# Kernel tuning notes

Hardware: AMD Instinct MI355X
Metric: run time of the kernel (lower is better)

## Reference

```python
import jax, jax.numpy as jnp
import numpy as np


def setup_inputs() -> dict:
    key = jax.random.key(0)
    N, E, LENGTH, DIM = 50000, 800000, 128, 128
    k1, k2, k3 = jax.random.split(key, 3)
    x = jax.random.normal(k1, (N, LENGTH), dtype=jnp.float32)
    edge_index = jax.random.randint(k2, (2, E), 0, N, dtype=jnp.int32)
    W = jax.random.normal(k3, (LENGTH, DIM), dtype=jnp.float32) / np.sqrt(LENGTH).astype(np.float32)
    b = jnp.zeros((DIM,), dtype=jnp.float32)
    return {"x": x, "edge_index": edge_index, "W": W, "b": b, "length": LENGTH, "dim": DIM}


def reference(x, edge_index, W, b, length, dim):
    # GCNConv(length, dim) with default add_self_loops + symmetric normalization,
    # then ReLU and softmax over the feature axis (dim=1).
    N = x.shape[0]
    src, dst = edge_index[0], edge_index[1]  # messages flow src -> dst (PyG source_to_target)
    loop = jnp.arange(N, dtype=src.dtype)
    src = jnp.concatenate([src, loop])
    dst = jnp.concatenate([dst, loop])
    # degree (incl. self-loops) computed on destination nodes, as in PyG gcn_norm
    deg = jax.ops.segment_sum(jnp.ones(dst.shape, dtype=x.dtype), dst, num_segments=N)
    dinv = jnp.where(deg > 0, jax.lax.rsqrt(deg), 0.0)
    norm = dinv[src] * dinv[dst]  # [E+N]
    xw = x @ W  # [N, dim] -- transform before propagate (in >= out here)
    msgs = xw[src] * norm[:, None]  # [E+N, dim] gather + scale
    out = jax.ops.segment_sum(msgs, dst, num_segments=N) + b  # scatter-add
    out = jax.nn.relu(out)
    return jax.nn.softmax(out, axis=1)
```

## Files before the change

### kernel.cpp

```cpp
#include <hip/hip_runtime.h>
#include <hip/hip_bf16.h>


#define KDIM 128
#define CAP 48

__device__ __forceinline__ unsigned short f2bf(float f) {
    union { float f; unsigned u; } v; v.f = f;
    unsigned r = v.u + 0x7fff + ((v.u >> 16) & 1);
    return (unsigned short)(r >> 16);
}
__device__ __forceinline__ float bflo(unsigned u) {
    union { unsigned u; float f; } v; v.u = u << 16; return v.f;
}
__device__ __forceinline__ float bfhi(unsigned u) {
    union { unsigned u; float f; } v; v.u = u & 0xffff0000u; return v.f;
}

__global__ __launch_bounds__(256) void fused_k(const float* __restrict__ x,
                                               const float* __restrict__ W,
                                               const int* __restrict__ src,
                                               const int* __restrict__ dst,
                                               int* __restrict__ degi,
                                               unsigned short* __restrict__ csr,
                                               unsigned short* __restrict__ xwh,
                                               int N, int E, int GB) {
    __shared__ float Xl[128 * 17];
    __shared__ float Wl[16 * 132];

    const int tid = threadIdx.x;

    if ((int)blockIdx.x >= GB) {
        int e = ((int)blockIdx.x - GB) * 256 + tid;
        if (e < E) {
            int d = dst[e];
            int s = src[e];
            int pos = atomicAdd(&degi[d], 1);
            if (pos < CAP) csr[d * CAP + pos] = (unsigned short)s;
        }
        return;
    }

    const int tx = tid & 15;
    const int ty = tid >> 4;
    const int rbase = (int)blockIdx.x * 128;

    float acc[8][8];
#pragma unroll
    for (int j = 0; j < 8; ++j)
#pragma unroll
        for (int c = 0; c < 8; ++c) acc[j][c] = 0.f;

    for (int kc = 0; kc < KDIM; kc += 16) {
#pragma unroll
        for (int i = 0; i < 2; ++i) {
            int p = tid + 256 * i;
            int row = p >> 2;
            int c4 = p & 3;
            int gr = rbase + row;
            float4 v = make_float4(0.f, 0.f, 0.f, 0.f);
            if (gr < N) v = *(const float4*)(&x[(size_t)gr * KDIM + kc + c4 * 4]);
            float* dp = &Xl[row * 17 + c4 * 4];
            dp[0] = v.x; dp[1] = v.y; dp[2] = v.z; dp[3] = v.w;
        }
#pragma unroll
        for (int i = 0; i < 2; ++i) {
            int p = tid + 256 * i;
            int k = p >> 5;
            int c4 = p & 31;
            float4 v = *(const float4*)(&W[(size_t)(kc + k) * KDIM + c4 * 4]);
            *(float4*)(&Wl[k * 132 + c4 * 4]) = v;
        }
        __syncthreads();

#pragma unroll
        for (int k = 0; k < 16; ++k) {
            float xr[8];
#pragma unroll
            for (int j = 0; j < 8; ++j) xr[j] = Xl[(ty * 8 + j) * 17 + k];
            float4 w0 = *(const float4*)(&Wl[k * 132 + tx * 4]);
            float4 w1 = *(const float4*)(&Wl[k * 132 + tx * 4 + 64]);
#pragma unroll
            for (int j = 0; j < 8; ++j) {
                acc[j][0] += xr[j] * w0.x; acc[j][1] += xr[j] * w0.y;
                acc[j][2] += xr[j] * w0.z; acc[j][3] += xr[j] * w0.w;
                acc[j][4] += xr[j] * w1.x; acc[j][5] += xr[j] * w1.y;
                acc[j][6] += xr[j] * w1.z; acc[j][7] += xr[j] * w1.w;
            }
        }
        __syncthreads();
    }

#pragma unroll
    for (int j = 0; j < 8; ++j) {
        int gr = rbase + ty * 8 + j;
        if (gr < N) {
            ushort4 o0, o1;
            o0.x = f2bf(acc[j][0]); o0.y = f2bf(acc[j][1]);
            o0.z = f2bf(acc[j][2]); o0.w = f2bf(acc[j][3]);
            o1.x = f2bf(acc[j][4]); o1.y = f2bf(acc[j][5]);
            o1.z = f2bf(acc[j][6]); o1.w = f2bf(acc[j][7]);
            *(ushort4*)(&xwh[(size_t)gr * KDIM + tx * 4]) = o0;
            *(ushort4*)(&xwh[(size_t)gr * KDIM + tx * 4 + 64]) = o1;
        }
    }
}

__global__ __launch_bounds__(256) void gather_k(const unsigned short* __restrict__ xwh,
                                                const unsigned short* __restrict__ csr,
                                                const int* __restrict__ degi,
                                                const float* __restrict__ b,
                                                float* __restrict__ out, int N) {
    int node = (blockIdx.x * blockDim.x + threadIdx.x) >> 6;
    if (node >= N) return;
    int lane = threadIdx.x & 63;
    int h = lane >> 4;
    int c = lane & 15;

    int cnt = degi[node];
    int ccnt = min(cnt, CAP);
    float dn = rsqrtf((float)(cnt + 1));

    float a[8];
#pragma unroll
    for (int i = 0; i < 8; ++i) a[i] = 0.f;

    if (h == 0) {
        float sn = dn * dn;
        uint4 u = *(const uint4*)(&xwh[(size_t)node * KDIM + c * 8]);
        float4 b0 = *(const float4*)(&b[c * 8]);
        float4 b1 = *(const float4*)(&b[c * 8 + 4]);
        a[0] = bflo(u.x) * sn + b0.x; a[1] = bfhi(u.x) * sn + b0.y;
        a[2] = bflo(u.y) * sn + b0.z; a[3] = bfhi(u.y) * sn + b0.w;
        a[4] = bflo(u.z) * sn + b1.x; a[5] = bfhi(u.z) * sn + b1.y;
        a[6] = bflo(u.w) * sn + b1.z; a[7] = bfhi(u.w) * sn + b1.w;
    }

    int s_l = 0;
    float w_l = 0.f;
    if (lane < ccnt) {
        s_l = csr[(size_t)node * CAP + lane];
        w_l = rsqrtf((float)(degi[s_l] + 1));
    }

    int kmax = (ccnt + 3) >> 2;
#pragma unroll 4
    for (int k = 0; k < kmax; ++k) {
        int idx = 4 * k + h;
        int s = __shfl(s_l, idx);
        float nv = __shfl(w_l, idx) * dn;
        uint4 u = *(const uint4*)(&xwh[(size_t)s * KDIM + c * 8]);
        a[0] += bflo(u.x) * nv; a[1] += bfhi(u.x) * nv;
        a[2] += bflo(u.y) * nv; a[3] += bfhi(u.y) * nv;
        a[4] += bflo(u.z) * nv; a[5] += bfhi(u.z) * nv;
        a[6] += bflo(u.w) * nv; a[7] += bfhi(u.w) * nv;
    }

#pragma unroll
    for (int off = 16; off <= 32; off <<= 1) {
#pragma unroll
        for (int i = 0; i < 8; ++i) a[i] += __shfl_xor(a[i], off);
    }

    float mx = -1e30f;
#pragma unroll
    for (int i = 0; i < 8; ++i) {
        a[i] = fmaxf(a[i], 0.f);
        mx = fmaxf(mx, a[i]);
    }
#pragma unroll
    for (int off = 1; off < 16; off <<= 1) mx = fmaxf(mx, __shfl_xor(mx, off));
    float e[8], s = 0.f;
#pragma unroll
    for (int i = 0; i < 8; ++i) {
        e[i] = __expf(a[i] - mx);
        s += e[i];
    }
#pragma unroll
    for (int off = 1; off < 16; off <<= 1) s += __shfl_xor(s, off);
    float rs = 1.0f / s;
    if (h == 0) {
        float4 o0 = make_float4(e[0] * rs, e[1] * rs, e[2] * rs, e[3] * rs);
        float4 o1 = make_float4(e[4] * rs, e[5] * rs, e[6] * rs, e[7] * rs);
        *(float4*)(&out[(size_t)node * KDIM + c * 8]) = o0;
        *(float4*)(&out[(size_t)node * KDIM + c * 8 + 4]) = o1;
    }
}

extern "C" void kernel_launch(void* const* d_in, const int* in_sizes, int n_in,
                              void* d_out, int out_size, void* d_ws, size_t ws_size,
                              hipStream_t stream) {
    const float* x  = (const float*)d_in[0];
    const int*   ei = (const int*)d_in[1];
    const float* W  = (const float*)d_in[2];
    const float* b  = (const float*)d_in[3];

    const int N = in_sizes[0] / KDIM;
    const int E = in_sizes[1] / 2;
    const int* src = ei;
    const int* dst = ei + E;

    unsigned short* xwh  = (unsigned short*)d_ws;
    int*            degi = (int*)(xwh + (size_t)N * KDIM);
    unsigned short* csr  = (unsigned short*)(degi + N);
    float*          out  = (float*)d_out;

    hipMemsetAsync(degi, 0, (size_t)N * sizeof(int), stream);

    const int GB = (N + 127) / 128;
    const int FB = (E + 255) / 256;
    fused_k<<<GB + FB, 256, 0, stream>>>(x, W, src, dst, degi, csr, xwh, N, E, GB);

    gather_k<<<(N + 3) / 4, 256, 0, stream>>>(xwh, csr, degi, b, out, N);
}
```

Before: 164.5 us.

## Use bf16 MFMA for the x@W transform instead of scalar FMA GEMM

Replaces the fp32 register-tiled SIMT GEMM with MFMA 16x16x32 bf16 instructions. W is converted to bf16 and stored transposed in LDS, and x fragments are loaded straight from global memory into registers and converted to bf16. The aim is to cut the compute cost of the dense transform, at the price of bf16 rounding on the inputs, scattered 2-byte LDS stores when staging W, and uncoalesced 2-byte output stores.

```diff
diff --git a/kernel.cpp b/kernel.cpp
--- a/kernel.cpp
+++ b/kernel.cpp
@@ -4,6 +4,9 @@
 
 #define KDIM 128
 #define CAP 48
+
+typedef __attribute__((ext_vector_type(8))) short bf16x8;
+typedef __attribute__((ext_vector_type(4))) float f32x4;
 
 __device__ __forceinline__ unsigned short f2bf(float f) {
     union { float f; unsigned u; } v; v.f = f;
@@ -16,6 +19,8 @@
 __device__ __forceinline__ float bfhi(unsigned u) {
     union { unsigned u; float f; } v; v.u = u & 0xffff0000u; return v.f;
 }
+
+#define WPAD 72
 
 __global__ __launch_bounds__(256) void fused_k(const float* __restrict__ x,
                                                const float* __restrict__ W,
@@ -25,8 +30,7 @@
                                                unsigned short* __restrict__ csr,
                                                unsigned short* __restrict__ xwh,
                                                int N, int E, int GB) {
-    __shared__ float Xl[128 * 17];
-    __shared__ float Wl[16 * 132];
+    __shared__ unsigned short Wl[128 * WPAD];
 
     const int tid = threadIdx.x;
 
@@ -41,67 +45,74 @@
         return;
     }
 
-    const int tx = tid & 15;
-    const int ty = tid >> 4;
+    const int lane = tid & 63;
+    const int wv = tid >> 6;
+    const int m15 = lane & 15;
+    const int quad = lane >> 4;
     const int rbase = (int)blockIdx.x * 128;
 
-    float acc[8][8];
-#pragma unroll
-    for (int j = 0; j < 8; ++j)
-#pragma unroll
-        for (int c = 0; c < 8; ++c) acc[j][c] = 0.f;
-
-    for (int kc = 0; kc < KDIM; kc += 16) {
-#pragma unroll
-        for (int i = 0; i < 2; ++i) {
+    f32x4 acc[2][8];
+#pragma unroll
+    for (int st = 0; st < 2; ++st)
+#pragma unroll
+        for (int nb = 0; nb < 8; ++nb) acc[st][nb] = (f32x4){0.f, 0.f, 0.f, 0.f};
+
+    for (int kc = 0; kc < KDIM; kc += 64) {
+#pragma unroll
+        for (int i = 0; i < 8; ++i) {
             int p = tid + 256 * i;
-            int row = p >> 2;
-            int c4 = p & 3;
-            int gr = rbase + row;
-            float4 v = make_float4(0.f, 0.f, 0.f, 0.f);
-            if (gr < N) v = *(const float4*)(&x[(size_t)gr * KDIM + kc + c4 * 4]);
-            float* dp = &Xl[row * 17 + c4 * 4];
-            dp[0] = v.x; dp[1] = v.y; dp[2] = v.z; dp[3] = v.w;
-        }
-#pragma unroll
-        for (int i = 0; i < 2; ++i) {
-            int p = tid + 256 * i;
-            int k = p >> 5;
+            int kk = p >> 5;
             int c4 = p & 31;
-            float4 v = *(const float4*)(&W[(size_t)(kc + k) * KDIM + c4 * 4]);
-            *(float4*)(&Wl[k * 132 + c4 * 4]) = v;
+            float4 v = *(const float4*)(&W[(size_t)(kc + kk) * KDIM + c4 * 4]);
+            int n0 = c4 * 4;
+            Wl[(n0 + 0) * WPAD + kk] = f2bf(v.x);
+            Wl[(n0 + 1) * WPAD + kk] = f2bf(v.y);
+            Wl[(n0 + 2) * WPAD + kk] = f2bf(v.z);
+            Wl[(n0 + 3) * WPAD + kk] = f2bf(v.w);
         }
         __syncthreads();
 
 #pragma unroll
-        for (int k = 0; k < 16; ++k) {
-            float xr[8];
-#pragma unroll
-            for (int j = 0; j < 8; ++j) xr[j] = Xl[(ty * 8 + j) * 17 + k];
-            float4 w0 = *(const float4*)(&Wl[k * 132 + tx * 4]);
-            float4 w1 = *(const float4*)(&Wl[k * 132 + tx * 4 + 64]);
-#pragma unroll
-            for (int j = 0; j < 8; ++j) {
-                acc[j][0] += xr[j] * w0.x; acc[j][1] += xr[j] * w0.y;
-                acc[j][2] += xr[j] * w0.z; acc[j][3] += xr[j] * w0.w;
-                acc[j][4] += xr[j] * w1.x; acc[j][5] += xr[j] * w1.y;
-                acc[j][6] += xr[j] * w1.z; acc[j][7] += xr[j] * w1.w;
+        for (int s2 = 0; s2 < 2; ++s2) {
+            int k0 = kc + s2 * 32 + quad * 8;
+            bf16x8 afr[2];
+#pragma unroll
+            for (int st = 0; st < 2; ++st) {
+                int gr = rbase + wv * 32 + st * 16 + m15;
+                int cr = min(gr, N - 1);
+                const float4* xp = (const float4*)(&x[(size_t)cr * KDIM + k0]);
+                float4 xa = xp[0], xb = xp[1];
+                bf16x8 f;
+                f[0] = (short)f2bf(xa.x); f[1] = (short)f2bf(xa.y);
+                f[2] = (short)f2bf(xa.z); f[3] = (short)f2bf(xa.w);
+                f[4] = (short)f2bf(xb.x); f[5] = (short)f2bf(xb.y);
+                f[6] = (short)f2bf(xb.z); f[7] = (short)f2bf(xb.w);
+                afr[st] = f;
             }
+            int kk0 = s2 * 32 + quad * 8;
+#pragma unroll
+            for (int nb = 0; nb < 8; ++nb) {
+                bf16x8 bfr = *(const bf16x8*)(&Wl[(nb * 16 + m15) * WPAD + kk0]);
+#pragma unroll
+                for (int st = 0; st < 2; ++st)
+                    acc[st][nb] = __builtin_amdgcn_mfma_f32_16x16x32_bf16(
+                        afr[st], bfr, acc[st][nb], 0, 0, 0);
+            }
         }
         __syncthreads();
     }
 
 #pragma unroll
-    for (int j = 0; j < 8; ++j) {
-        int gr = rbase + ty * 8 + j;
-        if (gr < N) {
-            ushort4 o0, o1;
-            o0.x = f2bf(acc[j][0]); o0.y = f2bf(acc[j][1]);
-            o0.z = f2bf(acc[j][2]); o0.w = f2bf(acc[j][3]);
-            o1.x = f2bf(acc[j][4]); o1.y = f2bf(acc[j][5]);
-            o1.z = f2bf(acc[j][6]); o1.w = f2bf(acc[j][7]);
-            *(ushort4*)(&xwh[(size_t)gr * KDIM + tx * 4]) = o0;
-            *(ushort4*)(&xwh[(size_t)gr * KDIM + tx * 4 + 64]) = o1;
+    for (int st = 0; st < 2; ++st) {
+        int rowbase = rbase + wv * 32 + st * 16 + quad * 4;
+#pragma unroll
+        for (int r = 0; r < 4; ++r) {
+            int gr = rowbase + r;
+            if (gr < N) {
+#pragma unroll
+                for (int nb = 0; nb < 8; ++nb)
+                    xwh[(size_t)gr * KDIM + nb * 16 + m15] = f2bf(acc[st][nb][r]);
+            }
         }
     }
 }
```

New measurement: 159.9 us. 1.03x faster.
